# Kernel optimization log

Measured on AMD Instinct MI355X. Metric: run time of the kernel, lower is better.

## Reference

```python
import jax, jax.numpy as jnp
import numpy as np

B, N, M, D = 16, 1024, 4096, 256

def setup_inputs() -> dict:
    key = jax.random.key(0)
    k1, k2 = jax.random.split(key)
    encode = jax.random.normal(k1, (B, N, D), dtype=jnp.float32)
    # Codebook initialized uniform(-1/M, 1/M) in the torch module; use normal-scaled
    # values of comparable magnitude for a non-degenerate test.
    templat = jax.random.uniform(k2, (M, D), dtype=jnp.float32, minval=-1.0 / M, maxval=1.0 / M)
    return {"encode": encode, "templat": templat}

def reference(encode, templat):
    # eval-mode forward: match(encode, sample=False), detach='encode'
    enc = jax.lax.stop_gradient(encode)
    # squared-L2 distance via the expansion used in the source
    # dist[b,n,m] = |e|^2 - 2 e.t + |t|^2
    e_sq = jnp.sum(enc * enc, axis=-1, keepdims=True)        # (B,N,1)
    t_sq = jnp.sum(templat * templat, axis=-1)                # (M,)
    cross = jnp.einsum('bnd,md->bnm', enc, templat)           # (B,N,M)
    logits = -(e_sq - 2.0 * cross + t_sq)                     # (B,N,M)
    # zsoft = softmax(logits) computed in the module but only zidx/quant returned
    zidx = jnp.argmax(logits, axis=-1)                        # (B,N) int
    quant = templat[zidx]                                     # (B,N,D) gather
    return quant, zidx
```

## Files before the change

### kernel.cpp

```cpp
#include <hip/hip_runtime.h>


typedef _Float16 half8 __attribute__((ext_vector_type(8)));
typedef float f32x4 __attribute__((ext_vector_type(4)));

constexpr int B_ = 16, N_ = 1024, M_ = 4096, D_ = 256;
constexpr int ROWS = B_ * N_;
constexpr int BR = 128;
constexpr int BC = 128;
constexpr int NCT = 4;
constexpr int CS = 8;
constexpr int CPB = BC * NCT;
constexpr int KC = 32;
constexpr int NCH = NCT * (D_ / KC);
constexpr int LDH = 32;
constexpr int NPART = CS * 2;
constexpr float TSCALE = 131072.0f;
constexpr float INV2 = 1.52587890625e-05f;

__device__ __forceinline__ void gload16(const _Float16* g, _Float16* l) {
    __builtin_amdgcn_global_load_lds(
        (const __attribute__((address_space(1))) void*)g,
        (__attribute__((address_space(3))) void*)l, 16, 0, 0);
}

__global__ void split_kernel(const float* __restrict__ E, const float* __restrict__ T,
                             _Float16* __restrict__ Ehi, _Float16* __restrict__ Elo,
                             _Float16* __restrict__ Thi, _Float16* __restrict__ Tlo) {
    int idx = blockIdx.x * blockDim.x + threadIdx.x;
    int row = idx >> 5;
    int c8 = (idx & 31) * 8;
    if (row >= ROWS + M_) return;
    const float* src;
    _Float16 *hi, *lo;
    size_t off;
    float scale;
    if (row < ROWS) {
        off = (size_t)row * D_ + c8;
        src = E + off; hi = Ehi; lo = Elo; scale = 1.0f;
    } else {
        off = (size_t)(row - ROWS) * D_ + c8;
        src = T + off; hi = Thi; lo = Tlo; scale = TSCALE;
    }
    float x[8];
    *reinterpret_cast<float4*>(&x[0]) = *reinterpret_cast<const float4*>(src);
    *reinterpret_cast<float4*>(&x[4]) = *reinterpret_cast<const float4*>(src + 4);
    half8 h, l;
    #pragma unroll
    for (int j = 0; j < 8; j++) {
        float xs = x[j] * scale;
        _Float16 hh = (_Float16)xs;
        h[j] = hh;
        l[j] = (_Float16)(xs - (float)hh);
    }
    *reinterpret_cast<half8*>(hi + off) = h;
    *reinterpret_cast<half8*>(lo + off) = l;
}

__global__ void rowsq_kernel(const float* __restrict__ E, const float* __restrict__ T,
                             float* __restrict__ esq, float* __restrict__ tsq) {
    int gt = blockIdx.x * blockDim.x + threadIdx.x;
    int row = gt >> 4;
    int l = gt & 15;
    if (row >= ROWS + M_) return;
    const float* src = (row < ROWS) ? (E + (size_t)row * D_)
                                    : (T + (size_t)(row - ROWS) * D_);
    const float* p = src + (l >> 3) * 128 + (l & 7);
    float r = __fmul_rn(p[0], p[0]);
    #pragma unroll
    for (int i = 1; i < 16; i++) {
        float x = p[8 * i];
        r = __fadd_rn(r, __fmul_rn(x, x));
    }
    float u = __fadd_rn(r, __shfl_xor(r, 1, 64));
    float v = __fadd_rn(u, __shfl_xor(u, 2, 64));
    float w = __fadd_rn(v, __shfl_xor(v, 4, 64));
    float s = __fadd_rn(w, __shfl_xor(w, 8, 64));
    if (l == 0) {
        if (row < ROWS) esq[row] = s;
        else            tsq[row - ROWS] = s;
    }
}

__global__ __launch_bounds__(256, 4) void score_kernel(
    const _Float16* __restrict__ Ehi_g, const _Float16* __restrict__ Elo_g,
    const _Float16* __restrict__ Thi_g, const _Float16* __restrict__ Tlo_g,
    const float* __restrict__ esq, const float* __restrict__ tsq,
    float2* __restrict__ part) {
    __shared__ _Float16 Eh[BR][LDH];
    __shared__ _Float16 El[BR][LDH];
    __shared__ _Float16 Th[BC][LDH];
    __shared__ _Float16 Tl[BC][LDH];

    const int tid = threadIdx.x;
    const int w  = tid >> 6;
    const int l  = tid & 63;
    const int wr = w >> 1;
    const int wc = w & 1;
    const int q  = l >> 4;
    const int cl = l & 15;
    const int row0 = blockIdx.x * BR;
    const int cs = blockIdx.y;
    const int colB = cs * CPB;

    const int lrow = l >> 2;
    const int lk   = (l & 3) * 8;

    float best[16];
    int   bidx[16];
    #pragma unroll
    for (int i = 0; i < 16; i++) { best[i] = 3.4e38f; bidx[i] = 0; }

    f32x4 acc[4][4];

    for (int ch = 0; ch < NCH; ++ch) {
        const int ct = ch >> 3;
        const int kc = (ch & 7) * KC;
        if ((ch & 7) == 0) {
            #pragma unroll
            for (int i = 0; i < 4; i++)
                #pragma unroll
                for (int j = 0; j < 4; j++)
                    acc[i][j] = (f32x4){0.f, 0.f, 0.f, 0.f};
        }
        __syncthreads();
        {
            const size_t eb = (size_t)(row0 + 32 * w) * D_ + kc + lk;
            const size_t tb = (size_t)(colB + ct * BC + 32 * w) * D_ + kc + lk;
            #pragma unroll
            for (int i = 0; i < 2; i++) {
                const size_t go = (size_t)(16 * i + lrow) * D_;
                gload16(Ehi_g + eb + go, &Eh[32 * w + 16 * i][0]);
                gload16(Elo_g + eb + go, &El[32 * w + 16 * i][0]);
                gload16(Thi_g + tb + go, &Th[32 * w + 16 * i][0]);
                gload16(Tlo_g + tb + go, &Tl[32 * w + 16 * i][0]);
            }
        }
        __syncthreads();

        half8 ah[4], bh[4], tmp[4];
        #pragma unroll
        for (int f = 0; f < 4; f++)
            ah[f] = *reinterpret_cast<const half8*>(&Eh[wr * 64 + f * 16 + cl][q * 8]);
        #pragma unroll
        for (int f = 0; f < 4; f++)
            bh[f] = *reinterpret_cast<const half8*>(&Th[wc * 64 + f * 16 + cl][q * 8]);
        #pragma unroll
        for (int i = 0; i < 4; i++)
            #pragma unroll
            for (int j = 0; j < 4; j++)
                acc[i][j] = __builtin_amdgcn_mfma_f32_16x16x32_f16(ah[i], bh[j], acc[i][j], 0, 0, 0);
        #pragma unroll
        for (int f = 0; f < 4; f++)
            tmp[f] = *reinterpret_cast<const half8*>(&Tl[wc * 64 + f * 16 + cl][q * 8]);
        #pragma unroll
        for (int i = 0; i < 4; i++)
            #pragma unroll
            for (int j = 0; j < 4; j++)
                acc[i][j] = __builtin_amdgcn_mfma_f32_16x16x32_f16(ah[i], tmp[j], acc[i][j], 0, 0, 0);
        #pragma unroll
        for (int f = 0; f < 4; f++)
            tmp[f] = *reinterpret_cast<const half8*>(&El[wr * 64 + f * 16 + cl][q * 8]);
        #pragma unroll
        for (int i = 0; i < 4; i++)
            #pragma unroll
            for (int j = 0; j < 4; j++)
                acc[i][j] = __builtin_amdgcn_mfma_f32_16x16x32_f16(tmp[i], bh[j], acc[i][j], 0, 0, 0);

        if ((ch & 7) == 7) {
            const int col0 = colB + ct * BC;
            float tc4[4];
            #pragma unroll
            for (int fc = 0; fc < 4; fc++)
                tc4[fc] = tsq[col0 + wc * 64 + fc * 16 + cl];
            #pragma unroll
            for (int fr = 0; fr < 4; fr++)
                #pragma unroll
                for (int rg = 0; rg < 4; rg++) {
                    const float er = esq[row0 + wr * 64 + fr * 16 + q * 4 + rg];
                    const int s = fr * 4 + rg;
                    #pragma unroll
                    for (int fc = 0; fc < 4; fc++) {
                        const float c2 = acc[fr][fc][rg] * INV2;
                        const float d1 = __fsub_rn(er, c2);
                        const float d2 = __fadd_rn(d1, tc4[fc]);
                        if (d2 < best[s]) { best[s] = d2; bidx[s] = col0 + wc * 64 + fc * 16 + cl; }
                    }
                }
        }
    }

    #pragma unroll
    for (int s = 0; s < 16; s++) {
        float v = best[s]; int i = bidx[s];
        #pragma unroll
        for (int off = 1; off < 16; off <<= 1) {
            float ov = __shfl_xor(v, off, 64);
            int   oi = __shfl_xor(i, off, 64);
            if (ov < v || (ov == v && oi < i)) { v = ov; i = oi; }
        }
        if (cl == 0) {
            const int row = row0 + wr * 64 + (s >> 2) * 16 + q * 4 + (s & 3);
            part[(size_t)row * NPART + cs * 2 + wc] = make_float2(v, __int_as_float(i));
        }
    }
}

__global__ void gather_kernel(const float* __restrict__ T, const float2* __restrict__ part,
                              float* __restrict__ quant, float* __restrict__ zout) {
    int gt = blockIdx.x * blockDim.x + threadIdx.x;
    int w = gt >> 6, lane = gt & 63;
    if (w >= ROWS) return;
    float2 p = part[(size_t)w * NPART];
    float v = p.x; int idx = __float_as_int(p.y);
    #pragma unroll
    for (int c = 1; c < NPART; c++) {
        float2 q = part[(size_t)w * NPART + c];
        int qi = __float_as_int(q.y);
        if (q.x < v || (q.x == v && qi < idx)) { v = q.x; idx = qi; }
    }
    float4 t = *reinterpret_cast<const float4*>(T + (size_t)idx * D_ + lane * 4);
    *reinterpret_cast<float4*>(quant + (size_t)w * D_ + lane * 4) = t;
    if (lane == 0) zout[w] = (float)idx;
}

extern "C" void kernel_launch(void* const* d_in, const int* in_sizes, int n_in,
                              void* d_out, int out_size, void* d_ws, size_t ws_size,
                              hipStream_t stream) {
    const float* E = (const float*)d_in[0];
    const float* T = (const float*)d_in[1];
    float* quant = (float*)d_out;
    float* zout  = quant + (size_t)ROWS * D_;

    float* esq   = (float*)d_ws;
    float* tsq   = esq + ROWS;
    float2* part = (float2*)(tsq + M_);
    _Float16* Ehi = (_Float16*)(part + (size_t)ROWS * NPART);
    _Float16* Elo = Ehi + (size_t)ROWS * D_;
    _Float16* Thi = Elo + (size_t)ROWS * D_;
    _Float16* Tlo = Thi + (size_t)M_ * D_;

    hipLaunchKernelGGL(split_kernel, dim3((ROWS + M_) * 32 / 256), dim3(256), 0, stream,
                       E, T, Ehi, Elo, Thi, Tlo);
    hipLaunchKernelGGL(rowsq_kernel, dim3((ROWS + M_) * 16 / 256), dim3(256), 0, stream, E, T, esq, tsq);
    hipLaunchKernelGGL(score_kernel, dim3(ROWS / BR, CS), dim3(256), 0, stream,
                       Ehi, Elo, Thi, Tlo, esq, tsq, part);
    hipLaunchKernelGGL(gather_kernel, dim3(ROWS * 64 / 256), dim3(256), 0, stream, T, part, quant, zout);
}
```

Measured before the change: 167.6 us.

## Double-buffer LDS tiles to prefetch next chunk during MFMA compute

Doubles the shared-memory tiles so the async global-to-LDS loads for the next K chunk are issued before computing on the current buffer. This removes one of the two barriers per chunk and hides load latency behind the MFMA work. It also drops the min-blocks occupancy hint and reorders the epilogue and El fragment loads to reduce register pressure. The cost is double the LDS footprint, which may lower the number of resident blocks per CU.

Result: faster. 163.1 us (-2.7%).

```diff
diff --git a/kernel.cpp b/kernel.cpp
--- a/kernel.cpp
+++ b/kernel.cpp
@@ -82,15 +82,15 @@
     }
 }
 
-__global__ __launch_bounds__(256, 4) void score_kernel(
+__global__ __launch_bounds__(256) void score_kernel(
     const _Float16* __restrict__ Ehi_g, const _Float16* __restrict__ Elo_g,
     const _Float16* __restrict__ Thi_g, const _Float16* __restrict__ Tlo_g,
     const float* __restrict__ esq, const float* __restrict__ tsq,
     float2* __restrict__ part) {
-    __shared__ _Float16 Eh[BR][LDH];
-    __shared__ _Float16 El[BR][LDH];
-    __shared__ _Float16 Th[BC][LDH];
-    __shared__ _Float16 Tl[BC][LDH];
+    __shared__ _Float16 Eh[2][BR][LDH];
+    __shared__ _Float16 El[2][BR][LDH];
+    __shared__ _Float16 Th[2][BC][LDH];
+    __shared__ _Float16 Tl[2][BC][LDH];
 
     const int tid = threadIdx.x;
     const int w  = tid >> 6;
@@ -113,9 +113,26 @@
 
     f32x4 acc[4][4];
 
+    #define STAGE(b_, ch_)                                                      \
+        {                                                                       \
+            const int ct_ = (ch_) >> 3, kc_ = ((ch_) & 7) * KC;                 \
+            const size_t eb = (size_t)(row0 + 32 * w) * D_ + kc_ + lk;          \
+            const size_t tb = (size_t)(colB + ct_ * BC + 32 * w) * D_ + kc_ + lk; \
+            _Pragma("unroll")                                                   \
+            for (int i_ = 0; i_ < 2; i_++) {                                    \
+                const size_t go = (size_t)(16 * i_ + lrow) * D_;                \
+                gload16(Ehi_g + eb + go, &Eh[b_][32 * w + 16 * i_][0]);         \
+                gload16(Elo_g + eb + go, &El[b_][32 * w + 16 * i_][0]);         \
+                gload16(Thi_g + tb + go, &Th[b_][32 * w + 16 * i_][0]);         \
+                gload16(Tlo_g + tb + go, &Tl[b_][32 * w + 16 * i_][0]);         \
+            }                                                                   \
+        }
+
+    STAGE(0, 0);
+    __syncthreads();
+    int buf = 0;
+
     for (int ch = 0; ch < NCH; ++ch) {
-        const int ct = ch >> 3;
-        const int kc = (ch & 7) * KC;
         if ((ch & 7) == 0) {
             #pragma unroll
             for (int i = 0; i < 4; i++)
@@ -123,28 +140,15 @@
                 for (int j = 0; j < 4; j++)
                     acc[i][j] = (f32x4){0.f, 0.f, 0.f, 0.f};
         }
-        __syncthreads();
-        {
-            const size_t eb = (size_t)(row0 + 32 * w) * D_ + kc + lk;
-            const size_t tb = (size_t)(colB + ct * BC + 32 * w) * D_ + kc + lk;
-            #pragma unroll
-            for (int i = 0; i < 2; i++) {
-                const size_t go = (size_t)(16 * i + lrow) * D_;
-                gload16(Ehi_g + eb + go, &Eh[32 * w + 16 * i][0]);
-                gload16(Elo_g + eb + go, &El[32 * w + 16 * i][0]);
-                gload16(Thi_g + tb + go, &Th[32 * w + 16 * i][0]);
-                gload16(Tlo_g + tb + go, &Tl[32 * w + 16 * i][0]);
-            }
-        }
-        __syncthreads();
+        if (ch < NCH - 1) STAGE(buf ^ 1, ch + 1);
 
         half8 ah[4], bh[4], tmp[4];
         #pragma unroll
         for (int f = 0; f < 4; f++)
-            ah[f] = *reinterpret_cast<const half8*>(&Eh[wr * 64 + f * 16 + cl][q * 8]);
+            ah[f] = *reinterpret_cast<const half8*>(&Eh[buf][wr * 64 + f * 16 + cl][q * 8]);
         #pragma unroll
         for (int f = 0; f < 4; f++)
-            bh[f] = *reinterpret_cast<const half8*>(&Th[wc * 64 + f * 16 + cl][q * 8]);
+            bh[f] = *reinterpret_cast<const half8*>(&Th[buf][wc * 64 + f * 16 + cl][q * 8]);
         #pragma unroll
         for (int i = 0; i < 4; i++)
             #pragma unroll
@@ -152,42 +156,43 @@
                 acc[i][j] = __builtin_amdgcn_mfma_f32_16x16x32_f16(ah[i], bh[j], acc[i][j], 0, 0, 0);
         #pragma unroll
         for (int f = 0; f < 4; f++)
-            tmp[f] = *reinterpret_cast<const half8*>(&Tl[wc * 64 + f * 16 + cl][q * 8]);
+            tmp[f] = *reinterpret_cast<const half8*>(&Tl[buf][wc * 64 + f * 16 + cl][q * 8]);
         #pragma unroll
         for (int i = 0; i < 4; i++)
             #pragma unroll
             for (int j = 0; j < 4; j++)
                 acc[i][j] = __builtin_amdgcn_mfma_f32_16x16x32_f16(ah[i], tmp[j], acc[i][j], 0, 0, 0);
         #pragma unroll
-        for (int f = 0; f < 4; f++)
-            tmp[f] = *reinterpret_cast<const half8*>(&El[wr * 64 + f * 16 + cl][q * 8]);
-        #pragma unroll
-        for (int i = 0; i < 4; i++)
+        for (int i = 0; i < 4; i++) {
+            half8 t = *reinterpret_cast<const half8*>(&El[buf][wr * 64 + i * 16 + cl][q * 8]);
             #pragma unroll
             for (int j = 0; j < 4; j++)
-                acc[i][j] = __builtin_amdgcn_mfma_f32_16x16x32_f16(tmp[i], bh[j], acc[i][j], 0, 0, 0);
+                acc[i][j] = __builtin_amdgcn_mfma_f32_16x16x32_f16(t, bh[j], acc[i][j], 0, 0, 0);
+        }
 
         if ((ch & 7) == 7) {
+            const int ct = ch >> 3;
             const int col0 = colB + ct * BC;
-            float tc4[4];
-            #pragma unroll
-            for (int fc = 0; fc < 4; fc++)
-                tc4[fc] = tsq[col0 + wc * 64 + fc * 16 + cl];
-            #pragma unroll
-            for (int fr = 0; fr < 4; fr++)
+            #pragma unroll
+            for (int fc = 0; fc < 4; fc++) {
+                const int col = col0 + wc * 64 + fc * 16 + cl;
+                const float tc = tsq[col];
                 #pragma unroll
-                for (int rg = 0; rg < 4; rg++) {
-                    const float er = esq[row0 + wr * 64 + fr * 16 + q * 4 + rg];
-                    const int s = fr * 4 + rg;
+                for (int fr = 0; fr < 4; fr++)
                     #pragma unroll
-                    for (int fc = 0; fc < 4; fc++) {
+                    for (int rg = 0; rg < 4; rg++) {
+                        const float er = esq[row0 + wr * 64 + fr * 16 + q * 4 + rg];
                         const float c2 = acc[fr][fc][rg] * INV2;
                         const float d1 = __fsub_rn(er, c2);
-                        const float d2 = __fadd_rn(d1, tc4[fc]);
-                        if (d2 < best[s]) { best[s] = d2; bidx[s] = col0 + wc * 64 + fc * 16 + cl; }
+                        const float d2 = __fadd_rn(d1, tc);
+                        const int s = fr * 4 + rg;
+                        if (d2 < best[s]) { best[s] = d2; bidx[s] = col; }
                     }
-                }
-        }
+            }
+        }
+
+        __syncthreads();
+        buf ^= 1;
     }
 
     #pragma unroll
@@ -204,6 +209,7 @@
             part[(size_t)row * NPART + cs * 2 + wc] = make_float2(v, __int_as_float(i));
         }
     }
+    #undef STAGE
 }
 
 __global__ void gather_kernel(const float* __restrict__ T, const float2* __restrict__ part,
```
